# Kernel optimization log

Hardware: AMD Instinct MI355X
Metric: run time of the kernel (lower is better)

Reference implementation:

```python
import jax, jax.numpy as jnp
import numpy as np

D = 16          # u_emb_size
LAYER_NUM = 2   # CAN layer_num

def setup_inputs() -> dict:
    key = jax.random.key(0)
    k1, k2 = jax.random.split(key)
    B, N = 16384, 50
    user_emb = jax.random.normal(k1, (B, N, D), dtype=jnp.float32)
    # item side packs per-sample MLP params: [W0(d*d), b0(d), W1(d*d), b1(d)]
    item_emb = jax.random.normal(k2, (B, D * (D + 1) * LAYER_NUM), dtype=jnp.float32)
    return {"user_emb": user_emb, "item_emb": item_emb}

def reference(user_emb, item_emb):
    B = user_emb.shape[0]
    x = user_emb  # (B, N, D)
    off = 0
    for _ in range(LAYER_NUM):
        W = item_emb[:, off:off + D * D].reshape(B, D, D); off += D * D
        b = item_emb[:, off:off + D].reshape(B, 1, D);      off += D
        # per-sample batched matmul + bias + relu
        x = jax.nn.relu(jnp.einsum('bnd,bde->bne', x, W) + b)
    return x  # (B, N, D); is_seq=False, is_stacked=True -> return as-is
```

## Files before the change

### kernel.cpp

```cpp
#include <hip/hip_runtime.h>


#define CAN_D 16
#define CAN_N 50
#define CAN_PSTRIDE 544
#define WAVES_PER_BLOCK 4
#define XSTAGE 3328
#define PSTAGE 2304
#define SSTAGE (XSTAGE + PSTAGE)
#define YS 20

typedef __attribute__((ext_vector_type(8))) short short8;
typedef __attribute__((ext_vector_type(4))) float f32x4;
#define AS1 __attribute__((address_space(1)))
#define AS3 __attribute__((address_space(3)))

union ABFrag { int i[4]; short8 v; };

__device__ __forceinline__ int pack2(float lo, float hi) {
    unsigned short ua = __builtin_bit_cast(unsigned short, (__bf16)lo);
    unsigned short ub = __builtin_bit_cast(unsigned short, (__bf16)hi);
    return (int)((unsigned)ua | ((unsigned)ub << 16));
}

__device__ __forceinline__ void dma16(const float* g, char* l) {
    __builtin_amdgcn_global_load_lds((const AS1 void*)g, (AS3 void*)l, 16, 0, 0);
}
__device__ __forceinline__ void dma4(const float* g, char* l) {
    __builtin_amdgcn_global_load_lds((const AS1 void*)g, (AS3 void*)l, 4, 0, 0);
}

__global__ __launch_bounds__(256, 5) void can_kernel(
    const float* __restrict__ user_emb,
    const float* __restrict__ item_emb,
    float* __restrict__ out, int B)
{
    __shared__ __align__(16) char smem[WAVES_PER_BLOCK * SSTAGE];

    const int wave = threadIdx.x >> 6;
    const int lane = threadIdx.x & 63;
    const int s = blockIdx.x * WAVES_PER_BLOCK + wave;
    const bool active = (s < B);

    char* xw = smem + wave * SSTAGE;
    char* pw = xw + XSTAGE;

    if (active) {
        const float* gx = user_emb + (size_t)s * (CAN_N * CAN_D);
        const float* gp = item_emb + (size_t)s * CAN_PSTRIDE;
        dma16(gx +       lane * 4, xw);
        dma16(gx + 256 + lane * 4, xw + 1024);
        dma16(gx + 512 + lane * 4, xw + 2048);
        { int idx = 768 + lane; if (idx > 799) idx = 799;
          dma4(gx + idx, xw + 3072); }
        dma16(gp +       lane * 4, pw);
        dma16(gp + 256 + lane * 4, pw + 1024);
        { int idx = 512 + lane; if (idx > 543) idx = 543;
          dma4(gp + idx, pw + 2048); }
    }

    __syncthreads();
    if (!active) return;

    const int n    = lane & 15;
    const int quad = lane >> 4;
    const float* pf = (const float*)pw;
    const float* xf = (const float*)xw;

    ABFrag w0, w1;
    const float b0v = pf[256 + n];
    const float b1v = pf[528 + n];
    if (quad < 2) {
        float t0[8], t1[8];
#pragma unroll
        for (int j = 0; j < 8; ++j) {
            t0[j] = pf[(quad * 8 + j) * CAN_D + n];
            t1[j] = pf[272 + (quad * 8 + j) * CAN_D + n];
        }
#pragma unroll
        for (int j = 0; j < 4; ++j) {
            w0.i[j] = pack2(t0[2 * j], t0[2 * j + 1]);
            w1.i[j] = pack2(t1[2 * j], t1[2 * j + 1]);
        }
    } else {
#pragma unroll
        for (int j = 0; j < 4; ++j) { w0.i[j] = 0; w1.i[j] = 0; }
    }

    ABFrag a0[4];
#pragma unroll
    for (int t = 0; t < 4; ++t) {
        if (quad < 2) {
            int row = t * 16 + n;
            if (row > CAN_N - 1) row = CAN_N - 1;
            const float4* pr = (const float4*)(xf + row * CAN_D + quad * 8);
            float4 u0 = pr[0], u1 = pr[1];
            a0[t].i[0] = pack2(u0.x, u0.y);
            a0[t].i[1] = pack2(u0.z, u0.w);
            a0[t].i[2] = pack2(u1.x, u1.y);
            a0[t].i[3] = pack2(u1.z, u1.w);
        } else {
#pragma unroll
            for (int j = 0; j < 4; ++j) a0[t].i[j] = 0;
        }
    }

    float* ob = out + (size_t)s * (CAN_N * CAN_D);

#pragma unroll
    for (int t = 0; t < 4; ++t) {
        float* yt = (float*)(xw + (t & 1) * 1280);

        f32x4 c0 = {b0v, b0v, b0v, b0v};
        c0 = __builtin_amdgcn_mfma_f32_16x16x32_bf16(a0[t].v, w0.v, c0, 0, 0, 0);

#pragma unroll
        for (int r = 0; r < 4; ++r)
            yt[(quad * 4 + r) * YS + n] = fmaxf(c0[r], 0.0f);

        ABFrag a1;
        if (quad < 2) {
            const float* pr = yt + n * YS + quad * 8;
            float4 v0 = *(const float4*)pr;
            float4 v1 = *(const float4*)(pr + 4);
            a1.i[0] = pack2(v0.x, v0.y);
            a1.i[1] = pack2(v0.z, v0.w);
            a1.i[2] = pack2(v1.x, v1.y);
            a1.i[3] = pack2(v1.z, v1.w);
        } else {
#pragma unroll
            for (int j = 0; j < 4; ++j) a1.i[j] = 0;
        }

        f32x4 c1 = {b1v, b1v, b1v, b1v};
        c1 = __builtin_amdgcn_mfma_f32_16x16x32_bf16(a1.v, w1.v, c1, 0, 0, 0);

#pragma unroll
        for (int r = 0; r < 4; ++r) {
            int grow = t * 16 + quad * 4 + r;
            if (grow < CAN_N)
                ob[grow * CAN_D + n] = fmaxf(c1[r], 0.0f);
        }
    }
}

extern "C" void kernel_launch(void* const* d_in, const int* in_sizes, int n_in,
                              void* d_out, int out_size, void* d_ws, size_t ws_size,
                              hipStream_t stream) {
    const float* user_emb = (const float*)d_in[0];
    const float* item_emb = (const float*)d_in[1];
    float* out = (float*)d_out;

    const int B = in_sizes[0] / (CAN_N * CAN_D);
    const int blocks = (B + WAVES_PER_BLOCK - 1) / WAVES_PER_BLOCK;
    can_kernel<<<blocks, 256, 0, stream>>>(user_emb, item_emb, out, B);
}
```

Baseline: 124.9 us.

## Use transposed 16x16x16 MFMA to chain layers in registers, load x directly

Switches from 16x16x32 bf16 MFMA with half the lanes zero-padded to 16x16x16 MFMA, computing the transposed product W^T·x^T. This puts each layer's output directly in the B-operand layout the second layer needs, so the LDS round trip for the intermediate is removed. User embeddings are now read straight from global memory as float4 per lane instead of staged through LDS, and outputs are written as float4. The smaller LDS footprint allows raising the launch bound to 8 blocks per SM, trading LDS staging for direct, possibly less coalesced global loads.

Result: no change. 124.5 us (-0.3%).

```diff
diff --git a/kernel.cpp b/kernel.cpp
--- a/kernel.cpp
+++ b/kernel.cpp
@@ -5,17 +5,14 @@
 #define CAN_N 50
 #define CAN_PSTRIDE 544
 #define WAVES_PER_BLOCK 4
-#define XSTAGE 3328
 #define PSTAGE 2304
-#define SSTAGE (XSTAGE + PSTAGE)
-#define YS 20
 
-typedef __attribute__((ext_vector_type(8))) short short8;
+typedef __attribute__((ext_vector_type(4))) short bf16x4;
 typedef __attribute__((ext_vector_type(4))) float f32x4;
 #define AS1 __attribute__((address_space(1)))
 #define AS3 __attribute__((address_space(3)))
 
-union ABFrag { int i[4]; short8 v; };
+union BFrag { int i[2]; bf16x4 v; };
 
 __device__ __forceinline__ int pack2(float lo, float hi) {
     unsigned short ua = __builtin_bit_cast(unsigned short, (__bf16)lo);
@@ -23,40 +20,42 @@
     return (int)((unsigned)ua | ((unsigned)ub << 16));
 }
 
-__device__ __forceinline__ void dma16(const float* g, char* l) {
-    __builtin_amdgcn_global_load_lds((const AS1 void*)g, (AS3 void*)l, 16, 0, 0);
-}
-__device__ __forceinline__ void dma4(const float* g, char* l) {
-    __builtin_amdgcn_global_load_lds((const AS1 void*)g, (AS3 void*)l, 4, 0, 0);
+__device__ __forceinline__ f32x4 mfma16(bf16x4 a, bf16x4 b, f32x4 c) {
+#if __has_builtin(__builtin_amdgcn_mfma_f32_16x16x16bf16_1k)
+    return __builtin_amdgcn_mfma_f32_16x16x16bf16_1k(a, b, c, 0, 0, 0);
+#else
+    f32x4 d;
+    asm volatile("s_nop 1\n\t"
+                 "v_mfma_f32_16x16x16_bf16 %0, %1, %2, %3\n\t"
+                 "s_nop 7\n\ts_nop 7"
+                 : "=&v"(d) : "v"(a), "v"(b), "v"(c));
+    return d;
+#endif
 }
 
-__global__ __launch_bounds__(256, 5) void can_kernel(
+__global__ __launch_bounds__(256, 8) void can_kernel(
     const float* __restrict__ user_emb,
     const float* __restrict__ item_emb,
     float* __restrict__ out, int B)
 {
-    __shared__ __align__(16) char smem[WAVES_PER_BLOCK * SSTAGE];
+    __shared__ __align__(16) char smem[WAVES_PER_BLOCK * PSTAGE];
 
     const int wave = threadIdx.x >> 6;
     const int lane = threadIdx.x & 63;
     const int s = blockIdx.x * WAVES_PER_BLOCK + wave;
     const bool active = (s < B);
 
-    char* xw = smem + wave * SSTAGE;
-    char* pw = xw + XSTAGE;
+    char* pw = smem + wave * PSTAGE;
 
     if (active) {
-        const float* gx = user_emb + (size_t)s * (CAN_N * CAN_D);
         const float* gp = item_emb + (size_t)s * CAN_PSTRIDE;
-        dma16(gx +       lane * 4, xw);
-        dma16(gx + 256 + lane * 4, xw + 1024);
-        dma16(gx + 512 + lane * 4, xw + 2048);
-        { int idx = 768 + lane; if (idx > 799) idx = 799;
-          dma4(gx + idx, xw + 3072); }
-        dma16(gp +       lane * 4, pw);
-        dma16(gp + 256 + lane * 4, pw + 1024);
-        { int idx = 512 + lane; if (idx > 543) idx = 543;
-          dma4(gp + idx, pw + 2048); }
+        __builtin_amdgcn_global_load_lds((const AS1 void*)(gp + lane * 4),
+                                         (AS3 void*)pw, 16, 0, 0);
+        __builtin_amdgcn_global_load_lds((const AS1 void*)(gp + 256 + lane * 4),
+                                         (AS3 void*)(pw + 1024), 16, 0, 0);
+        int idx = 512 + lane; if (idx > 543) idx = 543;
+        __builtin_amdgcn_global_load_lds((const AS1 void*)(gp + idx),
+                                         (AS3 void*)(pw + 2048), 4, 0, 0);
     }
 
     __syncthreads();
@@ -65,82 +64,48 @@
     const int n    = lane & 15;
     const int quad = lane >> 4;
     const float* pf = (const float*)pw;
-    const float* xf = (const float*)xw;
 
-    ABFrag w0, w1;
-    const float b0v = pf[256 + n];
-    const float b1v = pf[528 + n];
-    if (quad < 2) {
-        float t0[8], t1[8];
-#pragma unroll
-        for (int j = 0; j < 8; ++j) {
-            t0[j] = pf[(quad * 8 + j) * CAN_D + n];
-            t1[j] = pf[272 + (quad * 8 + j) * CAN_D + n];
-        }
+    BFrag w0, w1;
+    {
+        float t0[4], t1[4];
 #pragma unroll
         for (int j = 0; j < 4; ++j) {
-            w0.i[j] = pack2(t0[2 * j], t0[2 * j + 1]);
-            w1.i[j] = pack2(t1[2 * j], t1[2 * j + 1]);
+            t0[j] = pf[(4 * quad + j) * CAN_D + n];
+            t1[j] = pf[272 + (4 * quad + j) * CAN_D + n];
         }
-    } else {
-#pragma unroll
-        for (int j = 0; j < 4; ++j) { w0.i[j] = 0; w1.i[j] = 0; }
+        w0.i[0] = pack2(t0[0], t0[1]); w0.i[1] = pack2(t0[2], t0[3]);
+        w1.i[0] = pack2(t1[0], t1[1]); w1.i[1] = pack2(t1[2], t1[3]);
     }
+    const f32x4 b0v = *(const f32x4*)(pf + 256 + 4 * quad);
+    const f32x4 b1v = *(const f32x4*)(pf + 528 + 4 * quad);
 
-    ABFrag a0[4];
-#pragma unroll
-    for (int t = 0; t < 4; ++t) {
-        if (quad < 2) {
-            int row = t * 16 + n;
-            if (row > CAN_N - 1) row = CAN_N - 1;
-            const float4* pr = (const float4*)(xf + row * CAN_D + quad * 8);
-            float4 u0 = pr[0], u1 = pr[1];
-            a0[t].i[0] = pack2(u0.x, u0.y);
-            a0[t].i[1] = pack2(u0.z, u0.w);
-            a0[t].i[2] = pack2(u1.x, u1.y);
-            a0[t].i[3] = pack2(u1.z, u1.w);
-        } else {
-#pragma unroll
-            for (int j = 0; j < 4; ++j) a0[t].i[j] = 0;
-        }
-    }
-
+    const float* gx = user_emb + (size_t)s * (CAN_N * CAN_D);
     float* ob = out + (size_t)s * (CAN_N * CAN_D);
 
 #pragma unroll
     for (int t = 0; t < 4; ++t) {
-        float* yt = (float*)(xw + (t & 1) * 1280);
+        int row = t * 16 + n;
+        if (row > CAN_N - 1) row = CAN_N - 1;
+        f32x4 xv = *(const f32x4*)(gx + row * CAN_D + 4 * quad);
+        BFrag xb;
+        xb.i[0] = pack2(xv[0], xv[1]);
+        xb.i[1] = pack2(xv[2], xv[3]);
 
-        f32x4 c0 = {b0v, b0v, b0v, b0v};
-        c0 = __builtin_amdgcn_mfma_f32_16x16x32_bf16(a0[t].v, w0.v, c0, 0, 0, 0);
+        f32x4 d1 = mfma16(w0.v, xb.v, b0v);
 
+        BFrag yb;
+        yb.i[0] = pack2(fmaxf(d1[0], 0.0f), fmaxf(d1[1], 0.0f));
+        yb.i[1] = pack2(fmaxf(d1[2], 0.0f), fmaxf(d1[3], 0.0f));
+
+        f32x4 d2 = mfma16(w1.v, yb.v, b1v);
+
+        f32x4 r;
 #pragma unroll
-        for (int r = 0; r < 4; ++r)
-            yt[(quad * 4 + r) * YS + n] = fmaxf(c0[r], 0.0f);
+        for (int k = 0; k < 4; ++k) r[k] = fmaxf(d2[k], 0.0f);
 
-        ABFrag a1;
-        if (quad < 2) {
-            const float* pr = yt + n * YS + quad * 8;
-            float4 v0 = *(const float4*)pr;
-            float4 v1 = *(const float4*)(pr + 4);
-            a1.i[0] = pack2(v0.x, v0.y);
-            a1.i[1] = pack2(v0.z, v0.w);
-            a1.i[2] = pack2(v1.x, v1.y);
-            a1.i[3] = pack2(v1.z, v1.w);
-        } else {
-#pragma unroll
-            for (int j = 0; j < 4; ++j) a1.i[j] = 0;
-        }
-
-        f32x4 c1 = {b1v, b1v, b1v, b1v};
-        c1 = __builtin_amdgcn_mfma_f32_16x16x32_bf16(a1.v, w1.v, c1, 0, 0, 0);
-
-#pragma unroll
-        for (int r = 0; r < 4; ++r) {
-            int grow = t * 16 + quad * 4 + r;
-            if (grow < CAN_N)
-                ob[grow * CAN_D + n] = fmaxf(c1[r], 0.0f);
-        }
+        int orow = t * 16 + n;
+        if (orow < CAN_N)
+            *(f32x4*)(ob + orow * CAN_D + 4 * quad) = r;
     }
 }
 
```
